# Kernel tuning notes

Measured on AMD Instinct MI355X. Metric: run time of the kernel, lower is better.

Reference implementation:

```python
import jax, jax.numpy as jnp
import numpy as np

N = 100000
IN_CH = 128
OUT_CH = 128
E = 1600000


def setup_inputs() -> dict:
    key = jax.random.key(0)
    k1, k2, k3, k4 = jax.random.split(key, 4)
    x = jax.random.normal(k1, (N, IN_CH), dtype=jnp.float32)
    edge_index = jax.random.randint(k2, (2, E), 0, N, dtype=jnp.int64)
    # Glorot-style init for the GCNConv linear weight, zero bias (PyG default)
    W = jax.random.normal(k3, (IN_CH, OUT_CH), dtype=jnp.float32) * (1.0 / np.sqrt(IN_CH))
    b = jnp.zeros((OUT_CH,), dtype=jnp.float32)
    return {"x": x, "edge_index": edge_index, "W": W, "b": b}


def reference(x, edge_index, W, b):
    n = x.shape[0]
    # ---- add self loops (PyG GCNConv default add_self_loops=True) ----
    loops = jnp.arange(n, dtype=edge_index.dtype)
    row = jnp.concatenate([edge_index[0], loops])  # source
    col = jnp.concatenate([edge_index[1], loops])  # target
    # ---- symmetric degree normalization: D^{-1/2} (A+I) D^{-1/2} ----
    ones = jnp.ones(col.shape[0], dtype=x.dtype)
    deg = jax.ops.segment_sum(ones, col, num_segments=n)  # in-degree incl. self loop
    deg_inv_sqrt = jnp.where(deg > 0, jax.lax.rsqrt(deg), 0.0)
    norm = deg_inv_sqrt[row] * deg_inv_sqrt[col]  # [E+N]
    # ---- linear transform then gather-scale-scatter aggregation ----
    h = x @ W  # [N, OUT_CH]
    msgs = norm[:, None] * h[row]  # [E+N, OUT_CH]
    out = jax.ops.segment_sum(msgs, col, num_segments=n) + b  # [N, OUT_CH]
    # ---- ReLU ----
    return jax.nn.relu(out)
```

## Files before the change

kernel.cpp:

```cpp
#include <hip/hip_runtime.h>
#include <hip/hip_bf16.h>
#include <hip/hip_fp16.h>

#define IN_CH 128
#define OUT_CH 128
#define TM 64
#define CHUNK 8192
#define NPB 512
#define BSHIFT 9
#define CPAD 16
#define CAPT 16384

typedef __attribute__((ext_vector_type(8))) short short8;
typedef __attribute__((ext_vector_type(4))) float f32x4;
typedef __attribute__((ext_vector_type(2))) float f32x2;

__device__ __forceinline__ unsigned short f2bf(float f) {
    union { float f; unsigned u; } v; v.f = f;
    unsigned r = v.u + 0x7FFFu + ((v.u >> 16) & 1u);
    return (unsigned short)(r >> 16);
}


__global__ __launch_bounds__(256) void init_kernel(int* __restrict__ cursor, int NBK) {
    int t = threadIdx.x;
    if (t < NBK) cursor[t * CPAD] = t * CAPT;
}

__global__ __launch_bounds__(256) void partition_kernel(const int* __restrict__ row,
                                                        const int* __restrict__ col,
                                                        int* __restrict__ cursor,
                                                        int* __restrict__ tmp,
                                                        const float* __restrict__ W,
                                                        unsigned short* __restrict__ Wf,
                                                        int E, int NBK, int vec) {
    __shared__ int lcnt[256];
    __shared__ int lstart[256];
    __shared__ int lbase[256];
    __shared__ int lscan[256];
    __shared__ int buf[CHUNK];
    __shared__ unsigned char bid[CHUNK];
    int t = threadIdx.x;
    if (blockIdx.x == gridDim.x - 1) {
        for (int idx = t; idx < 16384; idx += 256) {
            int j = idx & 7;
            int lane = (idx >> 3) & 63;
            int ctks = idx >> 9;
            int ks = ctks & 3;
            int ct = ctks >> 2;
            int k = ks * 32 + (lane >> 4) * 8 + j;
            int nc = ct * 16 + (lane & 15);
            Wf[idx] = f2bf(W[k * 128 + nc]);
        }
        return;
    }
    int base = blockIdx.x * CHUNK;
    int nloc = min(CHUNK, E - base);
    lcnt[t] = 0;
    __syncthreads();
    if (vec) {
        const int4* c4 = (const int4*)(col + base);
        int nv = nloc >> 2;
        for (int i = t; i < nv; i += 256) {
            int4 c = c4[i];
            atomicAdd(&lcnt[c.x >> BSHIFT], 1);
            atomicAdd(&lcnt[c.y >> BSHIFT], 1);
            atomicAdd(&lcnt[c.z >> BSHIFT], 1);
            atomicAdd(&lcnt[c.w >> BSHIFT], 1);
        }
        for (int i = (nv << 2) + t; i < nloc; i += 256)
            atomicAdd(&lcnt[col[base + i] >> BSHIFT], 1);
    } else {
        for (int i = t; i < nloc; i += 256)
            atomicAdd(&lcnt[col[base + i] >> BSHIFT], 1);
    }
    __syncthreads();
    int v = lcnt[t];
    lscan[t] = v;
    __syncthreads();
    for (int off = 1; off < 256; off <<= 1) {
        int a = lscan[t];
        int b2 = (t >= off) ? lscan[t - off] : 0;
        __syncthreads();
        lscan[t] = a + b2;
        __syncthreads();
    }
    int excl = lscan[t] - v;
    lstart[t] = excl;
    lcnt[t] = excl;
    lbase[t] = (t < NBK && v) ? atomicAdd(&cursor[t * CPAD], v) : 0;
    __syncthreads();
    if (vec) {
        const int4* c4 = (const int4*)(col + base);
        const int4* r4 = (const int4*)(row + base);
        int nv = nloc >> 2;
        for (int i = t; i < nv; i += 256) {
            int4 c = c4[i];
            int4 r = r4[i];
            int b0 = c.x >> BSHIFT, p0 = atomicAdd(&lcnt[b0], 1);
            buf[p0] = r.x | ((c.x & (NPB - 1)) << 20); bid[p0] = (unsigned char)b0;
            int b1 = c.y >> BSHIFT, p1 = atomicAdd(&lcnt[b1], 1);
            buf[p1] = r.y | ((c.y & (NPB - 1)) << 20); bid[p1] = (unsigned char)b1;
            int b2 = c.z >> BSHIFT, p2 = atomicAdd(&lcnt[b2], 1);
            buf[p2] = r.z | ((c.z & (NPB - 1)) << 20); bid[p2] = (unsigned char)b2;
            int b3 = c.w >> BSHIFT, p3 = atomicAdd(&lcnt[b3], 1);
            buf[p3] = r.w | ((c.w & (NPB - 1)) << 20); bid[p3] = (unsigned char)b3;
        }
        for (int i = (nv << 2) + t; i < nloc; i += 256) {
            int c = col[base + i], r = row[base + i];
            int b = c >> BSHIFT, p = atomicAdd(&lcnt[b], 1);
            buf[p] = r | ((c & (NPB - 1)) << 20); bid[p] = (unsigned char)b;
        }
    } else {
        for (int i = t; i < nloc; i += 256) {
            int c = col[base + i], r = row[base + i];
            int b = c >> BSHIFT, p = atomicAdd(&lcnt[b], 1);
            buf[p] = r | ((c & (NPB - 1)) << 20); bid[p] = (unsigned char)b;
        }
    }
    __syncthreads();
    for (int i = t; i < nloc; i += 256) {
        int b = bid[i];
        int gidx = lbase[b] + (i - lstart[b]);
        if (gidx < (b + 1) * CAPT) tmp[gidx] = buf[i];
    }
}

__global__ __launch_bounds__(256) void csr_build_kernel(const int* __restrict__ tmp,
                                                        const int* __restrict__ cursor,
                                                        int* __restrict__ offs,
                                                        float* __restrict__ dis,
                                                        int* __restrict__ srcs,
                                                        int N, int NBK) {
    __shared__ int cnt[NPB];
    __shared__ int cur[NPB];
    __shared__ int bsum[256];
    int b = blockIdx.x;
    int t = threadIdx.x;
    int cv = (t < NBK) ? min(cursor[t * CPAD] - t * CAPT, CAPT) : 0;
    bsum[t] = cv;
    cnt[2 * t] = 0;
    cnt[2 * t + 1] = 0;
    __syncthreads();
    for (int off = 1; off < 256; off <<= 1) {
        int a = bsum[t];
        int b2 = (t >= off) ? bsum[t - off] : 0;
        __syncthreads();
        bsum[t] = a + b2;
        __syncthreads();
    }
    int wbeg = b * CAPT;
    int cnt_b = min(cursor[b * CPAD] - wbeg, CAPT);
    int cbeg = bsum[b] - cnt_b;
    if (b == 0 && t == 0) offs[N] = bsum[NBK - 1];
    for (int e = t; e < cnt_b; e += 256)
        atomicAdd(&cnt[(tmp[wbeg + e] >> 20)], 1);
    __syncthreads();
    int v0 = cnt[2 * t], v1 = cnt[2 * t + 1];
    int s = v0 + v1;
    cur[t] = s;
    __syncthreads();
    for (int off = 1; off < 256; off <<= 1) {
        int a = cur[t];
        int b2 = (t >= off) ? cur[t - off] : 0;
        __syncthreads();
        cur[t] = a + b2;
        __syncthreads();
    }
    int excl_pair = cur[t] - s;
    __syncthreads();
    int e0 = excl_pair;
    int e1 = excl_pair + v0;
    cur[2 * t] = e0;
    cur[2 * t + 1] = e1;
    int n0 = b * NPB + 2 * t;
    int n1 = n0 + 1;
    if (n0 < N) { offs[n0] = cbeg + e0; dis[n0] = rsqrtf((float)(v0 + 1)); }
    if (n1 < N) { offs[n1] = cbeg + e1; dis[n1] = rsqrtf((float)(v1 + 1)); }
    __syncthreads();
    for (int e = t; e < cnt_b; e += 256) {
        int p = tmp[wbeg + e];
        int slot = atomicAdd(&cur[p >> 20], 1);
        srcs[cbeg + slot] = p & 0xFFFFF;
    }
}

__global__ __launch_bounds__(256) void gemm_mfma_kernel(const float* __restrict__ A,
        const unsigned short* __restrict__ Wf, const float* __restrict__ dis,
        __half* __restrict__ G, int n) {
    int t = threadIdx.x;
    int w = t >> 6;
    int lane = t & 63;
    int m = lane & 15;
    int quad = lane >> 4;
    int row = blockIdx.x * TM + w * 16 + m;
    short8 af[4];
    if (row < n) {
        const f32x4* Ar = (const f32x4*)(A + (size_t)row * 128);
#pragma unroll
        for (int ks = 0; ks < 4; ++ks) {
            f32x4 v0 = __builtin_nontemporal_load(Ar + ks * 8 + quad * 2);
            f32x4 v1 = __builtin_nontemporal_load(Ar + ks * 8 + quad * 2 + 1);
            short8 a;
            a[0] = (short)f2bf(v0.x); a[1] = (short)f2bf(v0.y);
            a[2] = (short)f2bf(v0.z); a[3] = (short)f2bf(v0.w);
            a[4] = (short)f2bf(v1.x); a[5] = (short)f2bf(v1.y);
            a[6] = (short)f2bf(v1.z); a[7] = (short)f2bf(v1.w);
            af[ks] = a;
        }
    } else {
#pragma unroll
        for (int ks = 0; ks < 4; ++ks) af[ks] = (short8)0;
    }
    int grow_base = blockIdx.x * TM + w * 16 + quad * 4;
    float dsc[4];
#pragma unroll
    for (int reg = 0; reg < 4; ++reg)
        dsc[reg] = (grow_base + reg < n) ? dis[grow_base + reg] : 0.f;
    const short8* B8 = (const short8*)Wf;
#pragma unroll
    for (int ct = 0; ct < 8; ++ct) {
        f32x4 acc = {0.f, 0.f, 0.f, 0.f};
#pragma unroll
        for (int ks = 0; ks < 4; ++ks) {
            short8 bf = B8[(ct * 4 + ks) * 64 + lane];
            acc = __builtin_amdgcn_mfma_f32_16x16x32_bf16(af[ks], bf, acc, 0, 0, 0);
        }
        int nc = ct * 16 + m;
#pragma unroll
        for (int reg = 0; reg < 4; ++reg) {
            int grow = grow_base + reg;
            if (grow < n)
                G[(size_t)grow * 128 + nc] = __float2half(dsc[reg] * acc[reg]);
        }
    }
}

__global__ __launch_bounds__(256) void gemm_g16_kernel(const float* __restrict__ A,
        const float* __restrict__ W, const float* __restrict__ dis,
        __half* __restrict__ G, int n) {
    __shared__ __half Wh[128 * 128];
    __shared__ float As[TM * 128];
    int t = threadIdx.x;
    const float4* W4 = (const float4*)W;
#pragma unroll
    for (int j = 0; j < 16; ++j) {
        int idx = t + 256 * j;
        float4 v = W4[idx];
        __half2 p0 = __floats2half2_rn(v.x, v.y);
        __half2 p1 = __floats2half2_rn(v.z, v.w);
        *(__half2*)&Wh[idx * 4]     = p0;
        *(__half2*)&Wh[idx * 4 + 2] = p1;
    }
    int row0 = blockIdx.x * TM;
    const float4* A4 = (const float4*)A;
#pragma unroll
    for (int j = 0; j < 8; ++j) {
        int idx = t + 256 * j;
        int r = idx >> 5;
        int c4 = idx & 31;
        int gr = row0 + r;
        float4 v = make_float4(0.f, 0.f, 0.f, 0.f);
        if (gr < n) v = A4[(size_t)gr * 32 + c4];
        *(float4*)&As[r * 128 + c4 * 4] = v;
    }
    __syncthreads();
    int tcol = t & 15;
    int trow = t >> 4;
    int cb = tcol * 8;
    float acc[4][8];
#pragma unroll
    for (int r = 0; r < 4; ++r)
#pragma unroll
        for (int c = 0; c < 8; ++c) acc[r][c] = 0.f;
    const float* Abase = &As[(trow * 4) * 128];
#pragma unroll 4
    for (int k = 0; k < 128; ++k) {
        float4 wv = *(const float4*)&Wh[k * 128 + cb];
        const __half2* wh = (const __half2*)&wv;
        float2 w01 = __half22float2(wh[0]);
        float2 w23 = __half22float2(wh[1]);
        float2 w45 = __half22float2(wh[2]);
        float2 w67 = __half22float2(wh[3]);
        float wreg[8] = {w01.x, w01.y, w23.x, w23.y, w45.x, w45.y, w67.x, w67.y};
#pragma unroll
        for (int r = 0; r < 4; ++r) {
            float a = Abase[r * 128 + k];
#pragma unroll
            for (int c = 0; c < 8; ++c) acc[r][c] = fmaf(a, wreg[c], acc[r][c]);
        }
    }
#pragma unroll
    for (int r = 0; r < 4; ++r) {
        int gr = row0 + trow * 4 + r;
        if (gr < n) {
            float dsc2 = dis[gr];
            __half2 o[4];
#pragma unroll
            for (int j = 0; j < 4; ++j)
                o[j] = __floats2half2_rn(dsc2 * acc[r][2 * j], dsc2 * acc[r][2 * j + 1]);
            *(float4*)&G[(size_t)gr * 128 + cb] = *(float4*)o;
        }
    }
}

__global__ __launch_bounds__(256) void aggregate_g16_kernel(
        const __half2* __restrict__ g2, const int* __restrict__ srcs,
        const int* __restrict__ offs, const float* __restrict__ dis,
        const float* __restrict__ bias, float2* __restrict__ out2, int n) {
    int gid = blockIdx.x * blockDim.x + threadIdx.x;
    int wid = gid >> 6;
    int lane = gid & 63;
    if (wid >= n) return;
    int beg = offs[wid];
    int end = offs[wid + 1];
    float di = dis[wid];
    float2 xi = __half22float2(g2[(size_t)wid * 64 + lane]);
    float accx = xi.x;
    float accy = xi.y;
    int e = beg;
    for (; e + 8 <= end; e += 8) {
        int s0 = __builtin_nontemporal_load(srcs + e);
        int s1 = __builtin_nontemporal_load(srcs + e + 1);
        int s2 = __builtin_nontemporal_load(srcs + e + 2);
        int s3 = __builtin_nontemporal_load(srcs + e + 3);
        int s4 = __builtin_nontemporal_load(srcs + e + 4);
        int s5 = __builtin_nontemporal_load(srcs + e + 5);
        int s6 = __builtin_nontemporal_load(srcs + e + 6);
        int s7 = __builtin_nontemporal_load(srcs + e + 7);
        float2 v0 = __half22float2(g2[(size_t)s0 * 64 + lane]);
        float2 v1 = __half22float2(g2[(size_t)s1 * 64 + lane]);
        float2 v2 = __half22float2(g2[(size_t)s2 * 64 + lane]);
        float2 v3 = __half22float2(g2[(size_t)s3 * 64 + lane]);
        float2 v4 = __half22float2(g2[(size_t)s4 * 64 + lane]);
        float2 v5 = __half22float2(g2[(size_t)s5 * 64 + lane]);
        float2 v6 = __half22float2(g2[(size_t)s6 * 64 + lane]);
        float2 v7 = __half22float2(g2[(size_t)s7 * 64 + lane]);
        accx += ((v0.x + v1.x) + (v2.x + v3.x)) + ((v4.x + v5.x) + (v6.x + v7.x));
        accy += ((v0.y + v1.y) + (v2.y + v3.y)) + ((v4.y + v5.y) + (v6.y + v7.y));
    }
    for (; e + 4 <= end; e += 4) {
        int s0 = __builtin_nontemporal_load(srcs + e);
        int s1 = __builtin_nontemporal_load(srcs + e + 1);
        int s2 = __builtin_nontemporal_load(srcs + e + 2);
        int s3 = __builtin_nontemporal_load(srcs + e + 3);
        float2 v0 = __half22float2(g2[(size_t)s0 * 64 + lane]);
        float2 v1 = __half22float2(g2[(size_t)s1 * 64 + lane]);
        float2 v2 = __half22float2(g2[(size_t)s2 * 64 + lane]);
        float2 v3 = __half22float2(g2[(size_t)s3 * 64 + lane]);
        accx += (v0.x + v1.x) + (v2.x + v3.x);
        accy += (v0.y + v1.y) + (v2.y + v3.y);
    }
    for (; e < end; ++e) {
        float2 v = __half22float2(g2[(size_t)__builtin_nontemporal_load(srcs + e) * 64 + lane]);
        accx += v.x;
        accy += v.y;
    }
    float2 bv = ((const float2*)bias)[lane];
    f32x2 r;
    r.x = fmaxf(fmaf(di, accx, bv.x), 0.f);
    r.y = fmaxf(fmaf(di, accy, bv.y), 0.f);
    __builtin_nontemporal_store(r, (f32x2*)&out2[(size_t)wid * 64 + lane]);
}

__global__ void count_kernel(const int* __restrict__ col, int* __restrict__ deg, int E) {
    int i = blockIdx.x * blockDim.x + threadIdx.x;
    if (i < E) atomicAdd(&deg[col[i]], 1);
}

__global__ void scan_block_kernel(const int* __restrict__ in, int* __restrict__ out,
                                  int* __restrict__ bsums, float* __restrict__ dis, int n) {
    __shared__ int lds[256];
    int t = threadIdx.x;
    int base = blockIdx.x * 1024;
    int v[4];
    int idx = base + t * 4;
#pragma unroll
    for (int j = 0; j < 4; ++j) v[j] = (idx + j < n) ? in[idx + j] : 0;
#pragma unroll
    for (int j = 0; j < 4; ++j)
        if (idx + j < n) dis[idx + j] = rsqrtf((float)(v[j] + 1));
    int sum = v[0] + v[1] + v[2] + v[3];
    lds[t] = sum;
    __syncthreads();
    for (int off = 1; off < 256; off <<= 1) {
        int a = lds[t];
        int bq = (t >= off) ? lds[t - off] : 0;
        __syncthreads();
        lds[t] = a + bq;
        __syncthreads();
    }
    int run = (t == 0) ? 0 : lds[t - 1];
    if (t == 255 && bsums) bsums[blockIdx.x] = lds[255];
#pragma unroll
    for (int j = 0; j < 4; ++j) {
        if (idx + j < n) out[idx + j] = run;
        run += v[j];
    }
}

__global__ void scan_sums_kernel(int* __restrict__ bsums, int nB) {
    __shared__ int lds[256];
    int t = threadIdx.x;
    lds[t] = (t < nB) ? bsums[t] : 0;
    __syncthreads();
    for (int off = 1; off < 256; off <<= 1) {
        int a = lds[t];
        int bq = (t >= off) ? lds[t - off] : 0;
        __syncthreads();
        lds[t] = a + bq;
        __syncthreads();
    }
    if (t < nB) bsums[t] = (t == 0) ? 0 : lds[t - 1];
}

__global__ void scan_add_kernel(int* __restrict__ offs, const int* __restrict__ bsums,
                                int n, int total) {
    int i = blockIdx.x * blockDim.x + threadIdx.x;
    if (i < n) offs[i] += bsums[i >> 10];
    if (i == 0) offs[n] = total;
}

__global__ void fill_kernel(const int* __restrict__ row, const int* __restrict__ col,
                            const int* __restrict__ offs, int* __restrict__ deg,
                            int* __restrict__ srcs, int E) {
    int i = blockIdx.x * blockDim.x + threadIdx.x;
    if (i < E) {
        int c = col[i];
        int old = atomicSub(&deg[c], 1);
        srcs[offs[c] + old - 1] = row[i];
    }
}

__global__ __launch_bounds__(256) void aggregate_f32_kernel(
        const float2* __restrict__ x2, const int* __restrict__ srcs,
        const int* __restrict__ offs, const float* __restrict__ dis,
        float2* __restrict__ out2, int n) {
    int gid = blockIdx.x * blockDim.x + threadIdx.x;
    int wid = gid >> 6;
    int lane = gid & 63;
    if (wid >= n) return;
    int beg = offs[wid];
    int end = offs[wid + 1];
    float di = dis[wid];
    float2 xi = x2[(size_t)wid * 64 + lane];
    float accx = di * xi.x;
    float accy = di * xi.y;
    for (int e = beg; e < end; ++e) {
        int s = srcs[e];
        float ds = dis[s];
        float2 xs = x2[(size_t)s * 64 + lane];
        accx = fmaf(ds, xs.x, accx);
        accy = fmaf(ds, xs.y, accy);
    }
    float2 r;
    r.x = di * accx;
    r.y = di * accy;
    out2[(size_t)wid * 64 + lane] = r;
}

__global__ __launch_bounds__(256) void gemm_inplace_kernel(float* __restrict__ io,
                                                           const float* __restrict__ W,
                                                           const float* __restrict__ bias, int n) {
    __shared__ float rowL[128];
    __shared__ float part[128];
    int t = threadIdx.x;
    int c = t & 127;
    int half = t >> 7;
    float w[64];
#pragma unroll
    for (int j = 0; j < 64; ++j) w[j] = W[(half * 64 + j) * 128 + c];
    float bv = bias[c];
    int kbase = half * 64;
    for (int r = blockIdx.x; r < n; r += gridDim.x) {
        if (t < 128) rowL[t] = io[(size_t)r * 128 + t];
        __syncthreads();
        float acc = 0.f;
#pragma unroll
        for (int j = 0; j < 64; ++j) acc = fmaf(rowL[kbase + j], w[j], acc);
        if (half) part[c] = acc;
        __syncthreads();
        if (!half) {
            float v = acc + part[c] + bv;
            io[(size_t)r * 128 + c] = fmaxf(v, 0.f);
        }
        __syncthreads();
    }
}

extern "C" void kernel_launch(void* const* d_in, const int* in_sizes, int n_in,
                              void* d_out, int out_size, void* d_ws, size_t ws_size,
                              hipStream_t stream) {
    const float* x  = (const float*)d_in[0];
    const int*   ei = (const int*)d_in[1];
    const float* W  = (const float*)d_in[2];
    const float* b  = (const float*)d_in[3];
    float* out = (float*)d_out;

    int N = in_sizes[0] / IN_CH;
    int E = in_sizes[1] / 2;
    const int* rowp = ei;
    const int* colp = ei + E;
    int NBK = (N + NPB - 1) >> BSHIFT;
    int tpb = 256;
    int nchunks = (E + CHUNK - 1) / CHUNK;

    char* p = (char*)d_ws;
    auto take = [&](size_t bytes) { char* q = p; p += (bytes + 255) & ~(size_t)255; return q; };
    int*    cursor = (int*)take((size_t)256 * CPAD * 4);
    int*    offs   = (int*)take((size_t)(N + 1) * 4);
    float*  dis    = (float*)take((size_t)N * 4);
    int*    srcs   = (int*)take((size_t)E * 4);
    __half* g      = (__half*)take((size_t)N * 128 * 2);
    unsigned short* Wf = (unsigned short*)take((size_t)16384 * 2);
    bool fast = (NBK <= 256) && ((size_t)(p - (char*)d_ws) <= ws_size) &&
                ((size_t)NBK * CAPT <= (size_t)out_size) && (N < (1 << 20)) &&
                ((size_t)E + NPB <= (size_t)CAPT * NBK);

    long long threads_agg = (long long)N * 64;
    int agg_blocks = (int)((threads_agg + tpb - 1) / tpb);

    if (fast) {
        int* tmp = (int*)d_out;
        int vec = (((uintptr_t)colp | (uintptr_t)rowp) & 15) == 0 ? 1 : 0;
        init_kernel<<<1, 256, 0, stream>>>(cursor, NBK);
        partition_kernel<<<nchunks + 1, 256, 0, stream>>>(rowp, colp, cursor, tmp, W, Wf, E, NBK, vec);
        csr_build_kernel<<<NBK, 256, 0, stream>>>(tmp, cursor, offs, dis, srcs, N, NBK);
        gemm_mfma_kernel<<<(N + TM - 1) / TM, 256, 0, stream>>>(x, Wf, dis, g, N);
        aggregate_g16_kernel<<<agg_blocks, tpb, 0, stream>>>(
            (const __half2*)g, srcs, offs, dis, b, (float2*)out, N);
    } else {
        char* q = (char*)d_ws;
        auto take2 = [&](size_t bytes) { char* r = q; q += (bytes + 255) & ~(size_t)255; return r; };
        int*    deg2   = (int*)take2((size_t)N * 4);
        int*    offs2  = (int*)take2((size_t)(N + 1) * 4);
        int*    bsums2 = (int*)take2(256 * 4);
        int*    srcs2  = (int*)take2((size_t)E * 4);
        float*  dis2   = (float*)take2((size_t)N * 4);
        __half* g2b    = (__half*)take2((size_t)N * 128 * 2);
        bool fits2 = ((size_t)(q - (char*)d_ws)) <= ws_size;
        hipMemsetAsync(deg2, 0, (size_t)N * 4, stream);
        count_kernel<<<(E + tpb - 1) / tpb, tpb, 0, stream>>>(colp, deg2, E);
        int nB = (N + 1023) / 1024;
        scan_block_kernel<<<nB, 256, 0, stream>>>(deg2, offs2, bsums2, dis2, N);
        scan_sums_kernel<<<1, 256, 0, stream>>>(bsums2, nB);
        scan_add_kernel<<<(N + tpb - 1) / tpb, tpb, 0, stream>>>(offs2, bsums2, N, E);
        fill_kernel<<<(E + tpb - 1) / tpb, tpb, 0, stream>>>(rowp, colp, offs2, deg2, srcs2, E);
        if (fits2) {
            gemm_g16_kernel<<<(N + TM - 1) / TM, 256, 0, stream>>>(x, W, dis2, g2b, N);
            aggregate_g16_kernel<<<agg_blocks, tpb, 0, stream>>>(
                (const __half2*)g2b, srcs2, offs2, dis2, b, (float2*)out, N);
        } else {
            aggregate_f32_kernel<<<agg_blocks, tpb, 0, stream>>>(
                (const float2*)x, srcs2, offs2, dis2, (float2*)out, N);
            gemm_inplace_kernel<<<2048, 256, 0, stream>>>(out, W, b, N);
        }
    }
}
```

Before: 236.8 us.

## Fuse GEMM into partition kernel and move source-degree scaling to aggregation

The source-side D^-1/2 scaling now happens in the aggregation kernel instead of the GEMM epilogue. That removes the GEMM's dependency on the degree vector, so GEMM blocks can run in the same launch as edge partitioning and overlap with it. The W conversion moves into a multi-block init kernel. In exchange, aggregation does an extra random gather of dis[src] per edge, and the nontemporal hints on srcs loads and output stores are dropped.

```diff
diff --git a/kernel.cpp b/kernel.cpp
--- a/kernel.cpp
+++ b/kernel.cpp
@@ -13,7 +13,6 @@
 
 typedef __attribute__((ext_vector_type(8))) short short8;
 typedef __attribute__((ext_vector_type(4))) float f32x4;
-typedef __attribute__((ext_vector_type(2))) float f32x2;
 
 __device__ __forceinline__ unsigned short f2bf(float f) {
     union { float f; unsigned u; } v; v.f = f;
@@ -22,18 +21,39 @@
 }
 
 
-__global__ __launch_bounds__(256) void init_kernel(int* __restrict__ cursor, int NBK) {
-    int t = threadIdx.x;
-    if (t < NBK) cursor[t * CPAD] = t * CAPT;
-}
-
-__global__ __launch_bounds__(256) void partition_kernel(const int* __restrict__ row,
+__global__ __launch_bounds__(256) void init_kernel(int* __restrict__ cursor,
+                                                   const float* __restrict__ W,
+                                                   unsigned short* __restrict__ Wf,
+                                                   int NBK) {
+    int t = threadIdx.x;
+    if (blockIdx.x == 0) {
+        if (t < NBK) cursor[t * CPAD] = t * CAPT;
+        return;
+    }
+    int base = (blockIdx.x - 1) * 2048;
+#pragma unroll
+    for (int rep = 0; rep < 8; ++rep) {
+        int idx = base + rep * 256 + t;
+        int j = idx & 7;
+        int lane = (idx >> 3) & 63;
+        int ctks = idx >> 9;
+        int ks = ctks & 3;
+        int ct = ctks >> 2;
+        int k = ks * 32 + (lane >> 4) * 8 + j;
+        int nc = ct * 16 + (lane & 15);
+        Wf[idx] = f2bf(W[k * 128 + nc]);
+    }
+}
+
+__global__ __launch_bounds__(256) void part_gemm_kernel(const int* __restrict__ row,
                                                         const int* __restrict__ col,
                                                         int* __restrict__ cursor,
                                                         int* __restrict__ tmp,
-                                                        const float* __restrict__ W,
-                                                        unsigned short* __restrict__ Wf,
-                                                        int E, int NBK, int vec) {
+                                                        const float* __restrict__ A,
+                                                        const unsigned short* __restrict__ Wf,
+                                                        __half* __restrict__ G,
+                                                        int E, int n, int NBK, int vec,
+                                                        int nchunks) {
     __shared__ int lcnt[256];
     __shared__ int lstart[256];
     __shared__ int lbase[256];
@@ -41,16 +61,48 @@
     __shared__ int buf[CHUNK];
     __shared__ unsigned char bid[CHUNK];
     int t = threadIdx.x;
-    if (blockIdx.x == gridDim.x - 1) {
-        for (int idx = t; idx < 16384; idx += 256) {
-            int j = idx & 7;
-            int lane = (idx >> 3) & 63;
-            int ctks = idx >> 9;
-            int ks = ctks & 3;
-            int ct = ctks >> 2;
-            int k = ks * 32 + (lane >> 4) * 8 + j;
-            int nc = ct * 16 + (lane & 15);
-            Wf[idx] = f2bf(W[k * 128 + nc]);
+    if (blockIdx.x >= nchunks) {
+        int gb = blockIdx.x - nchunks;
+        int w = t >> 6;
+        int lane = t & 63;
+        int m = lane & 15;
+        int quad = lane >> 4;
+        int rowi = gb * TM + w * 16 + m;
+        short8 af[4];
+        if (rowi < n) {
+            const f32x4* Ar = (const f32x4*)(A + (size_t)rowi * 128);
+#pragma unroll
+            for (int ks = 0; ks < 4; ++ks) {
+                f32x4 v0 = __builtin_nontemporal_load(Ar + ks * 8 + quad * 2);
+                f32x4 v1 = __builtin_nontemporal_load(Ar + ks * 8 + quad * 2 + 1);
+                short8 a;
+                a[0] = (short)f2bf(v0.x); a[1] = (short)f2bf(v0.y);
+                a[2] = (short)f2bf(v0.z); a[3] = (short)f2bf(v0.w);
+                a[4] = (short)f2bf(v1.x); a[5] = (short)f2bf(v1.y);
+                a[6] = (short)f2bf(v1.z); a[7] = (short)f2bf(v1.w);
+                af[ks] = a;
+            }
+        } else {
+#pragma unroll
+            for (int ks = 0; ks < 4; ++ks) af[ks] = (short8)0;
+        }
+        int grow_base = gb * TM + w * 16 + quad * 4;
+        const short8* B8 = (const short8*)Wf;
+#pragma unroll
+        for (int ct = 0; ct < 8; ++ct) {
+            f32x4 acc = {0.f, 0.f, 0.f, 0.f};
+#pragma unroll
+            for (int ks = 0; ks < 4; ++ks) {
+                short8 bf = B8[(ct * 4 + ks) * 64 + lane];
+                acc = __builtin_amdgcn_mfma_f32_16x16x32_bf16(af[ks], bf, acc, 0, 0, 0);
+            }
+            int nc = ct * 16 + m;
+#pragma unroll
+            for (int reg = 0; reg < 4; ++reg) {
+                int grow = grow_base + reg;
+                if (grow < n)
+                    G[(size_t)grow * 128 + nc] = __float2half(acc[reg]);
+            }
         }
         return;
     }
@@ -185,125 +237,6 @@
     }
 }
 
-__global__ __launch_bounds__(256) void gemm_mfma_kernel(const float* __restrict__ A,
-        const unsigned short* __restrict__ Wf, const float* __restrict__ dis,
-        __half* __restrict__ G, int n) {
-    int t = threadIdx.x;
-    int w = t >> 6;
-    int lane = t & 63;
-    int m = lane & 15;
-    int quad = lane >> 4;
-    int row = blockIdx.x * TM + w * 16 + m;
-    short8 af[4];
-    if (row < n) {
-        const f32x4* Ar = (const f32x4*)(A + (size_t)row * 128);
-#pragma unroll
-        for (int ks = 0; ks < 4; ++ks) {
-            f32x4 v0 = __builtin_nontemporal_load(Ar + ks * 8 + quad * 2);
-            f32x4 v1 = __builtin_nontemporal_load(Ar + ks * 8 + quad * 2 + 1);
-            short8 a;
-            a[0] = (short)f2bf(v0.x); a[1] = (short)f2bf(v0.y);
-            a[2] = (short)f2bf(v0.z); a[3] = (short)f2bf(v0.w);
-            a[4] = (short)f2bf(v1.x); a[5] = (short)f2bf(v1.y);
-            a[6] = (short)f2bf(v1.z); a[7] = (short)f2bf(v1.w);
-            af[ks] = a;
-        }
-    } else {
-#pragma unroll
-        for (int ks = 0; ks < 4; ++ks) af[ks] = (short8)0;
-    }
-    int grow_base = blockIdx.x * TM + w * 16 + quad * 4;
-    float dsc[4];
-#pragma unroll
-    for (int reg = 0; reg < 4; ++reg)
-        dsc[reg] = (grow_base + reg < n) ? dis[grow_base + reg] : 0.f;
-    const short8* B8 = (const short8*)Wf;
-#pragma unroll
-    for (int ct = 0; ct < 8; ++ct) {
-        f32x4 acc = {0.f, 0.f, 0.f, 0.f};
-#pragma unroll
-        for (int ks = 0; ks < 4; ++ks) {
-            short8 bf = B8[(ct * 4 + ks) * 64 + lane];
-            acc = __builtin_amdgcn_mfma_f32_16x16x32_bf16(af[ks], bf, acc, 0, 0, 0);
-        }
-        int nc = ct * 16 + m;
-#pragma unroll
-        for (int reg = 0; reg < 4; ++reg) {
-            int grow = grow_base + reg;
-            if (grow < n)
-                G[(size_t)grow * 128 + nc] = __float2half(dsc[reg] * acc[reg]);
-        }
-    }
-}
-
-__global__ __launch_bounds__(256) void gemm_g16_kernel(const float* __restrict__ A,
-        const float* __restrict__ W, const float* __restrict__ dis,
-        __half* __restrict__ G, int n) {
-    __shared__ __half Wh[128 * 128];
-    __shared__ float As[TM * 128];
-    int t = threadIdx.x;
-    const float4* W4 = (const float4*)W;
-#pragma unroll
-    for (int j = 0; j < 16; ++j) {
-        int idx = t + 256 * j;
-        float4 v = W4[idx];
-        __half2 p0 = __floats2half2_rn(v.x, v.y);
-        __half2 p1 = __floats2half2_rn(v.z, v.w);
-        *(__half2*)&Wh[idx * 4]     = p0;
-        *(__half2*)&Wh[idx * 4 + 2] = p1;
-    }
-    int row0 = blockIdx.x * TM;
-    const float4* A4 = (const float4*)A;
-#pragma unroll
-    for (int j = 0; j < 8; ++j) {
-        int idx = t + 256 * j;
-        int r = idx >> 5;
-        int c4 = idx & 31;
-        int gr = row0 + r;
-        float4 v = make_float4(0.f, 0.f, 0.f, 0.f);
-        if (gr < n) v = A4[(size_t)gr * 32 + c4];
-        *(float4*)&As[r * 128 + c4 * 4] = v;
-    }
-    __syncthreads();
-    int tcol = t & 15;
-    int trow = t >> 4;
-    int cb = tcol * 8;
-    float acc[4][8];
-#pragma unroll
-    for (int r = 0; r < 4; ++r)
-#pragma unroll
-        for (int c = 0; c < 8; ++c) acc[r][c] = 0.f;
-    const float* Abase = &As[(trow * 4) * 128];
-#pragma unroll 4
-    for (int k = 0; k < 128; ++k) {
-        float4 wv = *(const float4*)&Wh[k * 128 + cb];
-        const __half2* wh = (const __half2*)&wv;
-        float2 w01 = __half22float2(wh[0]);
-        float2 w23 = __half22float2(wh[1]);
-        float2 w45 = __half22float2(wh[2]);
-        float2 w67 = __half22float2(wh[3]);
-        float wreg[8] = {w01.x, w01.y, w23.x, w23.y, w45.x, w45.y, w67.x, w67.y};
-#pragma unroll
-        for (int r = 0; r < 4; ++r) {
-            float a = Abase[r * 128 + k];
-#pragma unroll
-            for (int c = 0; c < 8; ++c) acc[r][c] = fmaf(a, wreg[c], acc[r][c]);
-        }
-    }
-#pragma unroll
-    for (int r = 0; r < 4; ++r) {
-        int gr = row0 + trow * 4 + r;
-        if (gr < n) {
-            float dsc2 = dis[gr];
-            __half2 o[4];
-#pragma unroll
-            for (int j = 0; j < 4; ++j)
-                o[j] = __floats2half2_rn(dsc2 * acc[r][2 * j], dsc2 * acc[r][2 * j + 1]);
-            *(float4*)&G[(size_t)gr * 128 + cb] = *(float4*)o;
-        }
-    }
-}
-
 __global__ __launch_bounds__(256) void aggregate_g16_kernel(
         const __half2* __restrict__ g2, const int* __restrict__ srcs,
         const int* __restrict__ offs, const float* __restrict__ dis,
@@ -316,18 +249,14 @@
     int end = offs[wid + 1];
     float di = dis[wid];
     float2 xi = __half22float2(g2[(size_t)wid * 64 + lane]);
-    float accx = xi.x;
-    float accy = xi.y;
+    float accx = di * xi.x;
+    float accy = di * xi.y;
     int e = beg;
     for (; e + 8 <= end; e += 8) {
-        int s0 = __builtin_nontemporal_load(srcs + e);
-        int s1 = __builtin_nontemporal_load(srcs + e + 1);
-        int s2 = __builtin_nontemporal_load(srcs + e + 2);
-        int s3 = __builtin_nontemporal_load(srcs + e + 3);
-        int s4 = __builtin_nontemporal_load(srcs + e + 4);
-        int s5 = __builtin_nontemporal_load(srcs + e + 5);
-        int s6 = __builtin_nontemporal_load(srcs + e + 6);
-        int s7 = __builtin_nontemporal_load(srcs + e + 7);
+        int s0 = srcs[e],     s1 = srcs[e + 1], s2 = srcs[e + 2], s3 = srcs[e + 3];
+        int s4 = srcs[e + 4], s5 = srcs[e + 5], s6 = srcs[e + 6], s7 = srcs[e + 7];
+        float d0 = dis[s0], d1 = dis[s1], d2 = dis[s2], d3 = dis[s3];
+        float d4 = dis[s4], d5 = dis[s5], d6 = dis[s6], d7 = dis[s7];
         float2 v0 = __half22float2(g2[(size_t)s0 * 64 + lane]);
         float2 v1 = __half22float2(g2[(size_t)s1 * 64 + lane]);
         float2 v2 = __half22float2(g2[(size_t)s2 * 64 + lane]);
@@ -336,31 +265,105 @@
         float2 v5 = __half22float2(g2[(size_t)s5 * 64 + lane]);
         float2 v6 = __half22float2(g2[(size_t)s6 * 64 + lane]);
         float2 v7 = __half22float2(g2[(size_t)s7 * 64 + lane]);
-        accx += ((v0.x + v1.x) + (v2.x + v3.x)) + ((v4.x + v5.x) + (v6.x + v7.x));
-        accy += ((v0.y + v1.y) + (v2.y + v3.y)) + ((v4.y + v5.y) + (v6.y + v7.y));
+        float tx0 = fmaf(d0, v0.x, d1 * v1.x);
+        float tx1 = fmaf(d2, v2.x, d3 * v3.x);
+        float tx2 = fmaf(d4, v4.x, d5 * v5.x);
+        float tx3 = fmaf(d6, v6.x, d7 * v7.x);
+        accx += (tx0 + tx1) + (tx2 + tx3);
+        float ty0 = fmaf(d0, v0.y, d1 * v1.y);
+        float ty1 = fmaf(d2, v2.y, d3 * v3.y);
+        float ty2 = fmaf(d4, v4.y, d5 * v5.y);
+        float ty3 = fmaf(d6, v6.y, d7 * v7.y);
+        accy += (ty0 + ty1) + (ty2 + ty3);
     }
     for (; e + 4 <= end; e += 4) {
-        int s0 = __builtin_nontemporal_load(srcs + e);
-        int s1 = __builtin_nontemporal_load(srcs + e + 1);
-        int s2 = __builtin_nontemporal_load(srcs + e + 2);
-        int s3 = __builtin_nontemporal_load(srcs + e + 3);
+        int s0 = srcs[e], s1 = srcs[e + 1], s2 = srcs[e + 2], s3 = srcs[e + 3];
+        float d0 = dis[s0], d1 = dis[s1], d2 = dis[s2], d3 = dis[s3];
         float2 v0 = __half22float2(g2[(size_t)s0 * 64 + lane]);
         float2 v1 = __half22float2(g2[(size_t)s1 * 64 + lane]);
         float2 v2 = __half22float2(g2[(size_t)s2 * 64 + lane]);
         float2 v3 = __half22float2(g2[(size_t)s3 * 64 + lane]);
-        accx += (v0.x + v1.x) + (v2.x + v3.x);
-        accy += (v0.y + v1.y) + (v2.y + v3.y);
+        accx += fmaf(d0, v0.x, d1 * v1.x) + fmaf(d2, v2.x, d3 * v3.x);
+        accy += fmaf(d0, v0.y, d1 * v1.y) + fmaf(d2, v2.y, d3 * v3.y);
     }
     for (; e < end; ++e) {
-        float2 v = __half22float2(g2[(size_t)__builtin_nontemporal_load(srcs + e) * 64 + lane]);
-        accx += v.x;
-        accy += v.y;
+        int s = srcs[e];
+        float ds = dis[s];
+        float2 v = __half22float2(g2[(size_t)s * 64 + lane]);
+        accx = fmaf(ds, v.x, accx);
+        accy = fmaf(ds, v.y, accy);
     }
     float2 bv = ((const float2*)bias)[lane];
-    f32x2 r;
+    float2 r;
     r.x = fmaxf(fmaf(di, accx, bv.x), 0.f);
     r.y = fmaxf(fmaf(di, accy, bv.y), 0.f);
-    __builtin_nontemporal_store(r, (f32x2*)&out2[(size_t)wid * 64 + lane]);
+    out2[(size_t)wid * 64 + lane] = r;
+}
+
+__global__ __launch_bounds__(256) void gemm_g16_kernel(const float* __restrict__ A,
+        const float* __restrict__ W, __half* __restrict__ G, int n) {
+    __shared__ __half Wh[128 * 128];
+    __shared__ float As[TM * 128];
+    int t = threadIdx.x;
+    const float4* W4 = (const float4*)W;
+#pragma unroll
+    for (int j = 0; j < 16; ++j) {
+        int idx = t + 256 * j;
+        float4 v = W4[idx];
+        __half2 p0 = __floats2half2_rn(v.x, v.y);
+        __half2 p1 = __floats2half2_rn(v.z, v.w);
+        *(__half2*)&Wh[idx * 4]     = p0;
+        *(__half2*)&Wh[idx * 4 + 2] = p1;
+    }
+    int row0 = blockIdx.x * TM;
+    const float4* A4 = (const float4*)A;
+#pragma unroll
+    for (int j = 0; j < 8; ++j) {
+        int idx = t + 256 * j;
+        int r = idx >> 5;
+        int c4 = idx & 31;
+        int gr = row0 + r;
+        float4 v = make_float4(0.f, 0.f, 0.f, 0.f);
+        if (gr < n) v = A4[(size_t)gr * 32 + c4];
+        *(float4*)&As[r * 128 + c4 * 4] = v;
+    }
+    __syncthreads();
+    int tcol = t & 15;
+    int trow = t >> 4;
+    int cb = tcol * 8;
+    float acc[4][8];
+#pragma unroll
+    for (int r = 0; r < 4; ++r)
+#pragma unroll
+        for (int c = 0; c < 8; ++c) acc[r][c] = 0.f;
+    const float* Abase = &As[(trow * 4) * 128];
+#pragma unroll 4
+    for (int k = 0; k < 128; ++k) {
+        float4 wv = *(const float4*)&Wh[k * 128 + cb];
+        const __half2* wh = (const __half2*)&wv;
+        float2 w01 = __half22float2(wh[0]);
+        float2 w23 = __half22float2(wh[1]);
+        float2 w45 = __half22float2(wh[2]);
+        float2 w67 = __half22float2(wh[3]);
+        float wreg[8] = {w01.x, w01.y, w23.x, w23.y, w45.x, w45.y, w67.x, w67.y};
+#pragma unroll
+        for (int r = 0; r < 4; ++r) {
+            float a = Abase[r * 128 + k];
+#pragma unroll
+            for (int c = 0; c < 8; ++c) acc[r][c] = fmaf(a, wreg[c], acc[r][c]);
+        }
+    }
+#pragma unroll
+    for (int r = 0; r < 4; ++r) {
+        int gr = row0 + trow * 4 + r;
+        if (gr < n) {
+            __half2 o[4];
+#pragma unroll
+            for (int j = 0; j < 4; ++j)
+                o[j] = __floats2half2_rn(acc[r][2 * j], acc[r][2 * j + 1]);
+            *(float4*)&G[(size_t)gr * 128 + cb] = *(float4*)o;
+        }
+    }
 }
 
 __global__ void count_kernel(const int* __restrict__ col, int* __restrict__ deg, int E) {
@@ -504,6 +507,7 @@
     int NBK = (N + NPB - 1) >> BSHIFT;
     int tpb = 256;
     int nchunks = (E + CHUNK - 1) / CHUNK;
+    int gemmBlocks = (N + TM - 1) / TM;
 
     char* p = (char*)d_ws;
     auto take = [&](size_t bytes) { char* q = p; p += (bytes + 255) & ~(size_t)255; return q; };
@@ -523,10 +527,10 @@
     if (fast) {
         int* tmp = (int*)d_out;
         int vec = (((uintptr_t)colp | (uintptr_t)rowp) & 15) == 0 ? 1 : 0;
-        init_kernel<<<1, 256, 0, stream>>>(cursor, NBK);
-        partition_kernel<<<nchunks + 1, 256, 0, stream>>>(rowp, colp, cursor, tmp, W, Wf, E, NBK, vec);
+        init_kernel<<<9, 256, 0, stream>>>(cursor, W, Wf, NBK);
+        part_gemm_kernel<<<nchunks + gemmBlocks, 256, 0, stream>>>(
+            rowp, colp, cursor, tmp, x, Wf, g, E, N, NBK, vec, nchunks);
         csr_build_kernel<<<NBK, 256, 0, stream>>>(tmp, cursor, offs, dis, srcs, N, NBK);
-        gemm_mfma_kernel<<<(N + TM - 1) / TM, 256, 0, stream>>>(x, Wf, dis, g, N);
         aggregate_g16_kernel<<<agg_blocks, tpb, 0, stream>>>(
             (const __half2*)g, srcs, offs, dis, b, (float2*)out, N);
     } else {
@@ -547,7 +551,7 @@
         scan_add_kernel<<<(N + tpb - 1) / tpb, tpb, 0, stream>>>(offs2, bsums2, N, E);
         fill_kernel<<<(E + tpb - 1) / tpb, tpb, 0, stream>>>(rowp, colp, offs2, deg2, srcs2, E);
         if (fits2) {
-            gemm_g16_kernel<<<(N + TM - 1) / TM, 256, 0, stream>>>(x, W, dis2, g2b, N);
+            gemm_g16_kernel<<<(N + TM - 1) / TM, 256, 0, stream>>>(x, W, g2b, N);
             aggregate_g16_kernel<<<agg_blocks, tpb, 0, stream>>>(
                 (const __half2*)g2b, srcs2, offs2, dis2, b, (float2*)out, N);
         } else {
```

Measured after the change: 216.9 us. -8.4%, faster.
